# Kernel tuning notes

Measured on AMD Instinct MI355X. Metric: run time of the kernel, lower is better.

The kernel has to match this reference:

```python
import jax, jax.numpy as jnp
import numpy as np

# dims
B, S, IN, H = 8, 2048, 512, 512
# biophysical constants (from module defaults / buffers)
DT = 0.1
TAU_M, TAU_ADAPT = 20.0, 100.0
V_REST, V_THRESH, V_RESET = -65.0, -50.0, -65.0
ADAPT_A, ADAPT_B = 0.5, 0.1
E_NA, E_K, E_L = 50.0, -77.0, -54.4
# HH gate initial values (IonicCurrents lazy init)
M0, H0, N0 = 0.05, 0.6, 0.32


def setup_inputs() -> dict:
    key = jax.random.key(0)
    k1, k2 = jax.random.split(key)
    x = jax.random.normal(k1, (B, S, IN), dtype=jnp.float32)
    W = jax.random.normal(k2, (H, IN), dtype=jnp.float32) * 0.01  # SynapticPlasticity.weights
    return {
        "x": x,
        "W": W,
        "g_Na": jnp.float32(120.0),
        "g_K": jnp.float32(36.0),
        "g_L": jnp.float32(0.3),
    }


def reference(x, W, g_Na, g_K, g_L):
    """BiologicalSNNLayer.forward, first call (all internal states at init).

    post_spikes = psp0 = 0 and traces start at 0, so the STDP dw is exactly 0
    on this call; psp = 0*decay + syn_input = syn_input.
    """
    dt = jnp.float32(DT)
    # SynapticPlasticity forward output: F.linear(x, W)
    syn = jnp.einsum("bsi,hi->bsh", x, W)  # [B,S,H]
    psp = syn
    V = psp
    # Hodgkin-Huxley gating: one Euler step from initial gate values
    am = 0.1 * (V + 40.0) / (1.0 - jnp.exp(-(V + 40.0) / 10.0))
    bm = 4.0 * jnp.exp(-(V + 65.0) / 18.0)
    ah = 0.07 * jnp.exp(-(V + 65.0) / 20.0)
    bh = 1.0 / (1.0 + jnp.exp(-(V + 35.0) / 10.0))
    an = 0.01 * (V + 55.0) / (1.0 - jnp.exp(-(V + 55.0) / 10.0))
    bn = 0.125 * jnp.exp(-(V + 65.0) / 80.0)
    m = M0 + dt * (am * (1.0 - M0) - bm * M0)
    h = H0 + dt * (ah * (1.0 - H0) - bh * H0)
    n = N0 + dt * (an * (1.0 - N0) - bn * N0)
    I_ion = (
        g_Na * m ** 3 * h * (V - E_NA)
        + g_K * n ** 4 * (V - E_K)
        + g_L * (V - E_L)
    )
    # Adaptive LIF (all hidden_size neurons share params -> vectorized over last dim)
    I_in = I_ion + psp
    # v0 = V_REST, w0 = 0 -> dv = I_in * dt/tau_m
    v_new = V_REST + I_in * (dt / TAU_M)
    spike = (v_new >= V_THRESH).astype(jnp.float32)
    w_new = (ADAPT_A * (v_new - V_REST) + ADAPT_B * spike) * (dt / TAU_ADAPT)
    v_rs = jnp.where(spike > 0.5, jnp.float32(V_RESET), v_new)
    return spike, v_rs, w_new
```

## Files before the change

### kernel.cpp

```cpp
#include <hip/hip_runtime.h>
#include <hip/hip_bf16.h>
#include <math.h>

typedef __bf16 bf16x8 __attribute__((ext_vector_type(8)));
typedef float  f32x4  __attribute__((ext_vector_type(4)));

#define M_DIM 16384
#define N_DIM 512
#define K_DIM 512
#define TBL_N 1024

#define X_ELEMS ((long)M_DIM * K_DIM)
#define W_ELEMS ((long)N_DIM * K_DIM)
#define WS_NEED ((X_ELEMS + W_ELEMS) * 2)

__global__ __launch_bounds__(256)
void convert_kernel(const float* __restrict__ x, const float* __restrict__ W,
                    __bf16* __restrict__ xb, __bf16* __restrict__ wb)
{
    const long XN8 = X_ELEMS / 8;
    const long T8  = XN8 + W_ELEMS / 8;
    for (long i = (long)blockIdx.x * 256 + threadIdx.x; i < T8;
         i += (long)gridDim.x * 256) {
        const float* src;
        __bf16* dst;
        if (i < XN8) { src = x + i * 8;          dst = xb + i * 8; }
        else         { src = W + (i - XN8) * 8;  dst = wb + (i - XN8) * 8; }
        float4 a = *(const float4*)src;
        float4 b = *(const float4*)(src + 4);
        bf16x8 r;
        r[0] = (__bf16)a.x; r[1] = (__bf16)a.y; r[2] = (__bf16)a.z; r[3] = (__bf16)a.w;
        r[4] = (__bf16)b.x; r[5] = (__bf16)b.y; r[6] = (__bf16)b.z; r[7] = (__bf16)b.w;
        *(bf16x8*)dst = r;
    }
}

__device__ inline void gl_lds16(const __bf16* g, __bf16* l) {
    __builtin_amdgcn_global_load_lds(
        (const __attribute__((address_space(1))) void*)g,
        (__attribute__((address_space(3))) void*)l, 16, 0, 0);
}

__global__ __launch_bounds__(256, 4)
void gemm_hh_kernel(const __bf16* __restrict__ xb, const __bf16* __restrict__ wb,
                    const float* __restrict__ gNa_p, const float* __restrict__ gK_p,
                    const float* __restrict__ gL_p, float* __restrict__ out)
{
    __shared__ __bf16 sW[64 * 64];
    __shared__ __bf16 sX[128 * 64];
    __shared__ float  tbl[TBL_N + 1];

    const int tid = threadIdx.x;

    const int id   = blockIdx.x;
    const int xcd  = id & 7;
    const int slot = id >> 3;
    const int bm   = xcd * 16 + (slot >> 3);
    const int bn   = slot & 7;

    const int wv   = tid >> 6;
    const int ln   = tid & 63;
    const int lr   = ln & 15;
    const int quad = ln >> 4;

    const int rw  = ln >> 3;
    const int ch  = ln & 7;
    const int chx = (ch ^ rw) * 8;
    const __bf16* wSrc = wb + ((long)bn * 64 + 16 * wv + rw) * K_DIM + chx;
    const __bf16* xSrc = xb + ((long)bm * 128 + 32 * wv + rw) * K_DIM + chx;

    #pragma unroll
    for (int j = 0; j < 2; ++j)
        gl_lds16(wSrc + (long)(8 * j) * K_DIM, sW + (16 * wv + 8 * j) * 64);
    #pragma unroll
    for (int j = 0; j < 4; ++j)
        gl_lds16(xSrc + (long)(8 * j) * K_DIM, sX + (32 * wv + 8 * j) * 64);

    {
        const float gNa = *gNa_p, gK = *gK_p, gL = *gL_p;
        for (int i = tid; i <= TBL_N; i += 256) {
            const float V = -4.0f + (8.0f / TBL_N) * i;
            const float am = 0.1f * (V + 40.0f) / (1.0f - expf(-(V + 40.0f) * 0.1f));
            const float bm_ = 4.0f * expf(-(V + 65.0f) * (1.0f / 18.0f));
            const float ah = 0.07f * expf(-(V + 65.0f) * 0.05f);
            const float bh = 1.0f / (1.0f + expf(-(V + 35.0f) * 0.1f));
            const float an = 0.01f * (V + 55.0f) / (1.0f - expf(-(V + 55.0f) * 0.1f));
            const float bn_ = 0.125f * expf(-(V + 65.0f) * 0.0125f);
            const float m = 0.05f + 0.1f * (am * 0.95f - bm_ * 0.05f);
            const float h = 0.60f + 0.1f * (ah * 0.40f - bh * 0.60f);
            const float n = 0.32f + 0.1f * (an * 0.68f - bn_ * 0.32f);
            tbl[i] = gNa * m * m * m * h * (V - 50.0f)
                   + gK * (n * n) * (n * n) * (V + 77.0f)
                   + gL * (V + 54.4f) + V;
        }
    }
    __syncthreads();

    f32x4 acc[4][2] = {};

    for (int t = 0; t < 8; ++t) {
        #pragma unroll
        for (int kk = 0; kk < 2; ++kk) {
            const int cidx = quad + 4 * kk;
            const int sl   = (cidx ^ (lr & 7)) * 8;
            bf16x8 aw[4], bx[2];
            #pragma unroll
            for (int f = 0; f < 4; ++f)
                aw[f] = *(const bf16x8*)(sW + (f * 16 + lr) * 64 + sl);
            #pragma unroll
            for (int g = 0; g < 2; ++g)
                bx[g] = *(const bf16x8*)(sX + (32 * wv + g * 16 + lr) * 64 + sl);
            #pragma unroll
            for (int f = 0; f < 4; ++f)
                #pragma unroll
                for (int g = 0; g < 2; ++g)
                    acc[f][g] = __builtin_amdgcn_mfma_f32_16x16x32_bf16(
                        aw[f], bx[g], acc[f][g], 0, 0, 0);
        }
        if (t < 7) {
            __syncthreads();
            const int kt = (t + 1) * 64;
            #pragma unroll
            for (int j = 0; j < 2; ++j)
                gl_lds16(wSrc + (long)(8 * j) * K_DIM + kt, sW + (16 * wv + 8 * j) * 64);
            #pragma unroll
            for (int j = 0; j < 4; ++j)
                gl_lds16(xSrc + (long)(8 * j) * K_DIM + kt, sX + (32 * wv + 8 * j) * 64);
            __syncthreads();
        }
    }

    float* outS = out;
    float* outV = out + (long)M_DIM * N_DIM;
    float* outW = out + 2L * M_DIM * N_DIM;

    #pragma unroll
    for (int f = 0; f < 4; ++f) {
        const int gn4 = bn * 64 + f * 16 + quad * 4;
        #pragma unroll
        for (int g = 0; g < 2; ++g) {
            const long gm  = (long)bm * 128 + 32 * wv + g * 16 + lr;
            const long idx = gm * N_DIM + gn4;
            f32x4 vS, vV, vW;
            #pragma unroll
            for (int i = 0; i < 4; ++i) {
                const float V = acc[f][g][i];
                float u = (V + 4.0f) * (TBL_N / 8.0f);
                u = fminf(fmaxf(u, 0.0f), (float)TBL_N - 0.001f);
                const int   iu = (int)u;
                const float fr = u - (float)iu;
                const float I_in = tbl[iu] + fr * (tbl[iu + 1] - tbl[iu]);
                const float v_new = -65.0f + I_in * 0.005f;
                const float spike = (v_new >= -50.0f) ? 1.0f : 0.0f;
                vS[i] = spike;
                vW[i] = (0.5f * (v_new + 65.0f) + 0.1f * spike) * 0.001f;
                vV[i] = (spike > 0.5f) ? -65.0f : v_new;
            }
            *(f32x4*)(outS + idx) = vS;
            *(f32x4*)(outV + idx) = vV;
            *(f32x4*)(outW + idx) = vW;
        }
    }
}

#define BMf 64
#define BNf 128
#define LDSTf 72
typedef __bf16 bf16x4 __attribute__((ext_vector_type(4)));
__global__ __launch_bounds__(256, 4)
void snn_fallback_kernel(const float* __restrict__ x, const float* __restrict__ W,
                         const float* __restrict__ gNa_p, const float* __restrict__ gK_p,
                         const float* __restrict__ gL_p, float* __restrict__ out)
{
    __shared__ __bf16 sA[BMf * LDSTf];
    __shared__ __bf16 sB[BNf * LDSTf];
    __shared__ float  tbl[TBL_N + 1];

    const int tid = threadIdx.x;
    const int id   = blockIdx.x;
    const int xcd  = id & 7;
    const int slot = id >> 3;
    const int bm   = xcd * 32 + (slot >> 2);
    const int bn   = slot & 3;

    const int c4 = (tid & 15) * 4;
    const int r0 = tid >> 4;
    const float* xBase = x + (long)(bm * BMf + r0) * K_DIM + c4;
    const float* wBase = W + (long)(bn * BNf + r0) * K_DIM + c4;

    const int wave = tid >> 6;
    const int lane = tid & 63;
    const int wM   = (wave & 1) * 32;
    const int wN   = (wave >> 1) * 64;
    const int lr   = lane & 15;
    const int quad = lane >> 4;

    f32x4 acc[2][4] = {};
    float4 pa[4], pb[8];
    #pragma unroll
    for (int rr = 0; rr < 4; ++rr) pa[rr] = *(const float4*)(xBase + (long)rr * 16 * K_DIM);
    #pragma unroll
    for (int rr = 0; rr < 8; ++rr) pb[rr] = *(const float4*)(wBase + (long)rr * 16 * K_DIM);

    {
        const float gNa = *gNa_p, gK = *gK_p, gL = *gL_p;
        for (int i = tid; i <= TBL_N; i += 256) {
            const float V = -4.0f + (8.0f / TBL_N) * i;
            const float am = 0.1f * (V + 40.0f) / (1.0f - expf(-(V + 40.0f) * 0.1f));
            const float bm_ = 4.0f * expf(-(V + 65.0f) * (1.0f / 18.0f));
            const float ah = 0.07f * expf(-(V + 65.0f) * 0.05f);
            const float bh = 1.0f / (1.0f + expf(-(V + 35.0f) * 0.1f));
            const float an = 0.01f * (V + 55.0f) / (1.0f - expf(-(V + 55.0f) * 0.1f));
            const float bn_ = 0.125f * expf(-(V + 65.0f) * 0.0125f);
            const float m = 0.05f + 0.1f * (am * 0.95f - bm_ * 0.05f);
            const float h = 0.60f + 0.1f * (ah * 0.40f - bh * 0.60f);
            const float n = 0.32f + 0.1f * (an * 0.68f - bn_ * 0.32f);
            tbl[i] = gNa * m * m * m * h * (V - 50.0f)
                   + gK * (n * n) * (n * n) * (V + 77.0f)
                   + gL * (V + 54.4f) + V;
        }
    }

    for (int kt = 0; kt < K_DIM; kt += 64) {
        const int ktn = (kt + 64 < K_DIM) ? kt + 64 : kt;
        const float* xp = xBase + ktn;
        const float* wp = wBase + ktn;
        #pragma unroll
        for (int rr = 0; rr < 4; ++rr) {
            float4 v = pa[rr];
            pa[rr] = *(const float4*)(xp + (long)rr * 16 * K_DIM);
            bf16x4 b = { (__bf16)v.x, (__bf16)v.y, (__bf16)v.z, (__bf16)v.w };
            *(bf16x4*)(&sA[(r0 + rr * 16) * LDSTf + c4]) = b;
        }
        #pragma unroll
        for (int rr = 0; rr < 8; ++rr) {
            float4 v = pb[rr];
            pb[rr] = *(const float4*)(wp + (long)rr * 16 * K_DIM);
            bf16x4 b = { (__bf16)v.x, (__bf16)v.y, (__bf16)v.z, (__bf16)v.w };
            *(bf16x4*)(&sB[(r0 + rr * 16) * LDSTf + c4]) = b;
        }
        __syncthreads();
        #pragma unroll
        for (int ks = 0; ks < 64; ks += 32) {
            bf16x8 af[2], bfr[4];
            #pragma unroll
            for (int t = 0; t < 2; ++t)
                af[t]  = *(const bf16x8*)(&sA[(wM + t * 16 + lr) * LDSTf + ks + quad * 8]);
            #pragma unroll
            for (int t = 0; t < 4; ++t)
                bfr[t] = *(const bf16x8*)(&sB[(wN + t * 16 + lr) * LDSTf + ks + quad * 8]);
            #pragma unroll
            for (int mt = 0; mt < 2; ++mt)
                #pragma unroll
                for (int nt = 0; nt < 4; ++nt)
                    acc[mt][nt] = __builtin_amdgcn_mfma_f32_16x16x32_bf16(
                        af[mt], bfr[nt], acc[mt][nt], 0, 0, 0);
        }
        __syncthreads();
    }

    float* outS = out;
    float* outV = out + (long)M_DIM * N_DIM;
    float* outW = out + 2L * M_DIM * N_DIM;
    #pragma unroll
    for (int mt = 0; mt < 2; ++mt) {
        #pragma unroll
        for (int i = 0; i < 4; ++i) {
            const long gm = (long)bm * BMf + wM + mt * 16 + quad * 4 + i;
            #pragma unroll
            for (int nt = 0; nt < 4; ++nt) {
                const int gn = bn * BNf + wN + nt * 16 + lr;
                const float V = acc[mt][nt][i];
                float u = (V + 4.0f) * (TBL_N / 8.0f);
                u = fminf(fmaxf(u, 0.0f), (float)TBL_N - 0.001f);
                const int   iu = (int)u;
                const float f  = u - (float)iu;
                const float I_in = tbl[iu] + f * (tbl[iu + 1] - tbl[iu]);
                const float v_new = -65.0f + I_in * 0.005f;
                const float spike = (v_new >= -50.0f) ? 1.0f : 0.0f;
                const float w_new = (0.5f * (v_new + 65.0f) + 0.1f * spike) * 0.001f;
                const float v_rs  = (spike > 0.5f) ? -65.0f : v_new;
                const long idx = gm * N_DIM + gn;
                outS[idx] = spike; outV[idx] = v_rs; outW[idx] = w_new;
            }
        }
    }
}

extern "C" void kernel_launch(void* const* d_in, const int* in_sizes, int n_in,
                              void* d_out, int out_size, void* d_ws, size_t ws_size,
                              hipStream_t stream) {
    const float* x   = (const float*)d_in[0];
    const float* W   = (const float*)d_in[1];
    const float* gNa = (const float*)d_in[2];
    const float* gK  = (const float*)d_in[3];
    const float* gL  = (const float*)d_in[4];
    float* out = (float*)d_out;

    if (ws_size >= (size_t)WS_NEED) {
        __bf16* xb = (__bf16*)d_ws;
        __bf16* wb = xb + X_ELEMS;
        hipLaunchKernelGGL(convert_kernel, dim3(1024), dim3(256), 0, stream, x, W, xb, wb);
        hipLaunchKernelGGL(gemm_hh_kernel, dim3(1024), dim3(256), 0, stream,
                           xb, wb, gNa, gK, gL, out);
    } else {
        hipLaunchKernelGGL(snn_fallback_kernel, dim3(1024), dim3(256), 0, stream,
                           x, W, gNa, gK, gL, out);
    }
}
```

Measured before the change: 149.0 us.

## Fuse fp32-to-bf16 conversion into GEMM with register-prefetched loads

Drops the separate conversion kernel that wrote bf16 copies of x and W to the workspace. The GEMM now reads fp32 directly, keeps the next k-tile in registers while the current one is computed, and converts to bf16 on the way into LDS. This removes a full extra read and write pass over x and a second launch. In exchange each block reads twice as many bytes per tile, uses more registers for the prefetch buffers, and gives up the direct global-to-LDS load path.

Measured after the change: 178.8 us. 1.2x slower.

```diff
diff --git a/kernel.cpp b/kernel.cpp
--- a/kernel.cpp
+++ b/kernel.cpp
@@ -10,41 +10,17 @@
 #define K_DIM 512
 #define TBL_N 1024
 
-#define X_ELEMS ((long)M_DIM * K_DIM)
-#define W_ELEMS ((long)N_DIM * K_DIM)
-#define WS_NEED ((X_ELEMS + W_ELEMS) * 2)
-
-__global__ __launch_bounds__(256)
-void convert_kernel(const float* __restrict__ x, const float* __restrict__ W,
-                    __bf16* __restrict__ xb, __bf16* __restrict__ wb)
-{
-    const long XN8 = X_ELEMS / 8;
-    const long T8  = XN8 + W_ELEMS / 8;
-    for (long i = (long)blockIdx.x * 256 + threadIdx.x; i < T8;
-         i += (long)gridDim.x * 256) {
-        const float* src;
-        __bf16* dst;
-        if (i < XN8) { src = x + i * 8;          dst = xb + i * 8; }
-        else         { src = W + (i - XN8) * 8;  dst = wb + (i - XN8) * 8; }
-        float4 a = *(const float4*)src;
-        float4 b = *(const float4*)(src + 4);
-        bf16x8 r;
-        r[0] = (__bf16)a.x; r[1] = (__bf16)a.y; r[2] = (__bf16)a.z; r[3] = (__bf16)a.w;
-        r[4] = (__bf16)b.x; r[5] = (__bf16)b.y; r[6] = (__bf16)b.z; r[7] = (__bf16)b.w;
-        *(bf16x8*)dst = r;
-    }
-}
-
-__device__ inline void gl_lds16(const __bf16* g, __bf16* l) {
-    __builtin_amdgcn_global_load_lds(
-        (const __attribute__((address_space(1))) void*)g,
-        (__attribute__((address_space(3))) void*)l, 16, 0, 0);
+__device__ inline bf16x8 cvt8(float4 a, float4 b) {
+    bf16x8 r;
+    r[0] = (__bf16)a.x; r[1] = (__bf16)a.y; r[2] = (__bf16)a.z; r[3] = (__bf16)a.w;
+    r[4] = (__bf16)b.x; r[5] = (__bf16)b.y; r[6] = (__bf16)b.z; r[7] = (__bf16)b.w;
+    return r;
 }
 
 __global__ __launch_bounds__(256, 4)
-void gemm_hh_kernel(const __bf16* __restrict__ xb, const __bf16* __restrict__ wb,
-                    const float* __restrict__ gNa_p, const float* __restrict__ gK_p,
-                    const float* __restrict__ gL_p, float* __restrict__ out)
+void snn_fused_kernel(const float* __restrict__ x, const float* __restrict__ W,
+                      const float* __restrict__ gNa_p, const float* __restrict__ gK_p,
+                      const float* __restrict__ gL_p, float* __restrict__ out)
 {
     __shared__ __bf16 sW[64 * 64];
     __shared__ __bf16 sX[128 * 64];
@@ -66,15 +42,23 @@
     const int rw  = ln >> 3;
     const int ch  = ln & 7;
     const int chx = (ch ^ rw) * 8;
-    const __bf16* wSrc = wb + ((long)bn * 64 + 16 * wv + rw) * K_DIM + chx;
-    const __bf16* xSrc = xb + ((long)bm * 128 + 32 * wv + rw) * K_DIM + chx;
 
+    const float* wSrc = W + ((long)bn * 64 + 16 * wv + rw) * K_DIM + chx;
+    const float* xSrc = x + ((long)bm * 128 + 32 * wv + rw) * K_DIM + chx;
+    __bf16* wDst = sW + (16 * wv + rw) * 64 + ch * 8;
+    __bf16* xDst = sX + (32 * wv + rw) * 64 + ch * 8;
+
+    float4 pw[2][2], px[4][2];
     #pragma unroll
-    for (int j = 0; j < 2; ++j)
-        gl_lds16(wSrc + (long)(8 * j) * K_DIM, sW + (16 * wv + 8 * j) * 64);
+    for (int j = 0; j < 2; ++j) {
+        pw[j][0] = *(const float4*)(wSrc + (long)(8 * j) * K_DIM);
+        pw[j][1] = *(const float4*)(wSrc + (long)(8 * j) * K_DIM + 4);
+    }
     #pragma unroll
-    for (int j = 0; j < 4; ++j)
-        gl_lds16(xSrc + (long)(8 * j) * K_DIM, sX + (32 * wv + 8 * j) * 64);
+    for (int j = 0; j < 4; ++j) {
+        px[j][0] = *(const float4*)(xSrc + (long)(8 * j) * K_DIM);
+        px[j][1] = *(const float4*)(xSrc + (long)(8 * j) * K_DIM + 4);
+    }
 
     {
         const float gNa = *gNa_p, gK = *gK_p, gL = *gL_p;
@@ -94,11 +78,30 @@
                    + gL * (V + 54.4f) + V;
         }
     }
-    __syncthreads();
 
     f32x4 acc[4][2] = {};
 
     for (int t = 0; t < 8; ++t) {
+        const int nk = (t + 1) * 64;
+        #pragma unroll
+        for (int j = 0; j < 2; ++j) {
+            float4 a = pw[j][0], b = pw[j][1];
+            if (t < 7) {
+                pw[j][0] = *(const float4*)(wSrc + (long)(8 * j) * K_DIM + nk);
+                pw[j][1] = *(const float4*)(wSrc + (long)(8 * j) * K_DIM + nk + 4);
+            }
+            *(bf16x8*)(wDst + 8 * j * 64) = cvt8(a, b);
+        }
+        #pragma unroll
+        for (int j = 0; j < 4; ++j) {
+            float4 a = px[j][0], b = px[j][1];
+            if (t < 7) {
+                px[j][0] = *(const float4*)(xSrc + (long)(8 * j) * K_DIM + nk);
+                px[j][1] = *(const float4*)(xSrc + (long)(8 * j) * K_DIM + nk + 4);
+            }
+            *(bf16x8*)(xDst + 8 * j * 64) = cvt8(a, b);
+        }
+        __syncthreads();
         #pragma unroll
         for (int kk = 0; kk < 2; ++kk) {
             const int cidx = quad + 4 * kk;
@@ -117,17 +120,7 @@
                     acc[f][g] = __builtin_amdgcn_mfma_f32_16x16x32_bf16(
                         aw[f], bx[g], acc[f][g], 0, 0, 0);
         }
-        if (t < 7) {
-            __syncthreads();
-            const int kt = (t + 1) * 64;
-            #pragma unroll
-            for (int j = 0; j < 2; ++j)
-                gl_lds16(wSrc + (long)(8 * j) * K_DIM + kt, sW + (16 * wv + 8 * j) * 64);
-            #pragma unroll
-            for (int j = 0; j < 4; ++j)
-                gl_lds16(xSrc + (long)(8 * j) * K_DIM + kt, sX + (32 * wv + 8 * j) * 64);
-            __syncthreads();
-        }
+        __syncthreads();
     }
 
     float* outS = out;
@@ -163,130 +156,6 @@
     }
 }
 
-#define BMf 64
-#define BNf 128
-#define LDSTf 72
-typedef __bf16 bf16x4 __attribute__((ext_vector_type(4)));
-__global__ __launch_bounds__(256, 4)
-void snn_fallback_kernel(const float* __restrict__ x, const float* __restrict__ W,
-                         const float* __restrict__ gNa_p, const float* __restrict__ gK_p,
-                         const float* __restrict__ gL_p, float* __restrict__ out)
-{
-    __shared__ __bf16 sA[BMf * LDSTf];
-    __shared__ __bf16 sB[BNf * LDSTf];
-    __shared__ float  tbl[TBL_N + 1];
-
-    const int tid = threadIdx.x;
-    const int id   = blockIdx.x;
-    const int xcd  = id & 7;
-    const int slot = id >> 3;
-    const int bm   = xcd * 32 + (slot >> 2);
-    const int bn   = slot & 3;
-
-    const int c4 = (tid & 15) * 4;
-    const int r0 = tid >> 4;
-    const float* xBase = x + (long)(bm * BMf + r0) * K_DIM + c4;
-    const float* wBase = W + (long)(bn * BNf + r0) * K_DIM + c4;
-
-    const int wave = tid >> 6;
-    const int lane = tid & 63;
-    const int wM   = (wave & 1) * 32;
-    const int wN   = (wave >> 1) * 64;
-    const int lr   = lane & 15;
-    const int quad = lane >> 4;
-
-    f32x4 acc[2][4] = {};
-    float4 pa[4], pb[8];
-    #pragma unroll
-    for (int rr = 0; rr < 4; ++rr) pa[rr] = *(const float4*)(xBase + (long)rr * 16 * K_DIM);
-    #pragma unroll
-    for (int rr = 0; rr < 8; ++rr) pb[rr] = *(const float4*)(wBase + (long)rr * 16 * K_DIM);
-
-    {
-        const float gNa = *gNa_p, gK = *gK_p, gL = *gL_p;
-        for (int i = tid; i <= TBL_N; i += 256) {
-            const float V = -4.0f + (8.0f / TBL_N) * i;
-            const float am = 0.1f * (V + 40.0f) / (1.0f - expf(-(V + 40.0f) * 0.1f));
-            const float bm_ = 4.0f * expf(-(V + 65.0f) * (1.0f / 18.0f));
-            const float ah = 0.07f * expf(-(V + 65.0f) * 0.05f);
-            const float bh = 1.0f / (1.0f + expf(-(V + 35.0f) * 0.1f));
-            const float an = 0.01f * (V + 55.0f) / (1.0f - expf(-(V + 55.0f) * 0.1f));
-            const float bn_ = 0.125f * expf(-(V + 65.0f) * 0.0125f);
-            const float m = 0.05f + 0.1f * (am * 0.95f - bm_ * 0.05f);
-            const float h = 0.60f + 0.1f * (ah * 0.40f - bh * 0.60f);
-            const float n = 0.32f + 0.1f * (an * 0.68f - bn_ * 0.32f);
-            tbl[i] = gNa * m * m * m * h * (V - 50.0f)
-                   + gK * (n * n) * (n * n) * (V + 77.0f)
-                   + gL * (V + 54.4f) + V;
-        }
-    }
-
-    for (int kt = 0; kt < K_DIM; kt += 64) {
-        const int ktn = (kt + 64 < K_DIM) ? kt + 64 : kt;
-        const float* xp = xBase + ktn;
-        const float* wp = wBase + ktn;
-        #pragma unroll
-        for (int rr = 0; rr < 4; ++rr) {
-            float4 v = pa[rr];
-            pa[rr] = *(const float4*)(xp + (long)rr * 16 * K_DIM);
-            bf16x4 b = { (__bf16)v.x, (__bf16)v.y, (__bf16)v.z, (__bf16)v.w };
-            *(bf16x4*)(&sA[(r0 + rr * 16) * LDSTf + c4]) = b;
-        }
-        #pragma unroll
-        for (int rr = 0; rr < 8; ++rr) {
-            float4 v = pb[rr];
-            pb[rr] = *(const float4*)(wp + (long)rr * 16 * K_DIM);
-            bf16x4 b = { (__bf16)v.x, (__bf16)v.y, (__bf16)v.z, (__bf16)v.w };
-            *(bf16x4*)(&sB[(r0 + rr * 16) * LDSTf + c4]) = b;
-        }
-        __syncthreads();
-        #pragma unroll
-        for (int ks = 0; ks < 64; ks += 32) {
-            bf16x8 af[2], bfr[4];
-            #pragma unroll
-            for (int t = 0; t < 2; ++t)
-                af[t]  = *(const bf16x8*)(&sA[(wM + t * 16 + lr) * LDSTf + ks + quad * 8]);
-            #pragma unroll
-            for (int t = 0; t < 4; ++t)
-                bfr[t] = *(const bf16x8*)(&sB[(wN + t * 16 + lr) * LDSTf + ks + quad * 8]);
-            #pragma unroll
-            for (int mt = 0; mt < 2; ++mt)
-                #pragma unroll
-                for (int nt = 0; nt < 4; ++nt)
-                    acc[mt][nt] = __builtin_amdgcn_mfma_f32_16x16x32_bf16(
-                        af[mt], bfr[nt], acc[mt][nt], 0, 0, 0);
-        }
-        __syncthreads();
-    }
-
-    float* outS = out;
-    float* outV = out + (long)M_DIM * N_DIM;
-    float* outW = out + 2L * M_DIM * N_DIM;
-    #pragma unroll
-    for (int mt = 0; mt < 2; ++mt) {
-        #pragma unroll
-        for (int i = 0; i < 4; ++i) {
-            const long gm = (long)bm * BMf + wM + mt * 16 + quad * 4 + i;
-            #pragma unroll
-            for (int nt = 0; nt < 4; ++nt) {
-                const int gn = bn * BNf + wN + nt * 16 + lr;
-                const float V = acc[mt][nt][i];
-                float u = (V + 4.0f) * (TBL_N / 8.0f);
-                u = fminf(fmaxf(u, 0.0f), (float)TBL_N - 0.001f);
-                const int   iu = (int)u;
-                const float f  = u - (float)iu;
-                const float I_in = tbl[iu] + f * (tbl[iu + 1] - tbl[iu]);
-                const float v_new = -65.0f + I_in * 0.005f;
-                const float spike = (v_new >= -50.0f) ? 1.0f : 0.0f;
-                const float w_new = (0.5f * (v_new + 65.0f) + 0.1f * spike) * 0.001f;
-                const float v_rs  = (spike > 0.5f) ? -65.0f : v_new;
-                const long idx = gm * N_DIM + gn;
-                outS[idx] = spike; outV[idx] = v_rs; outW[idx] = w_new;
-            }
-        }
-    }
-}
-
 extern "C" void kernel_launch(void* const* d_in, const int* in_sizes, int n_in,
                               void* d_out, int out_size, void* d_ws, size_t ws_size,
                               hipStream_t stream) {
@@ -296,15 +165,8 @@
     const float* gK  = (const float*)d_in[3];
     const float* gL  = (const float*)d_in[4];
     float* out = (float*)d_out;
+    (void)d_ws; (void)ws_size;
 
-    if (ws_size >= (size_t)WS_NEED) {
-        __bf16* xb = (__bf16*)d_ws;
-        __bf16* wb = xb + X_ELEMS;
-        hipLaunchKernelGGL(convert_kernel, dim3(1024), dim3(256), 0, stream, x, W, xb, wb);
-        hipLaunchKernelGGL(gemm_hh_kernel, dim3(1024), dim3(256), 0, stream,
-                           xb, wb, gNa, gK, gL, out);
-    } else {
-        hipLaunchKernelGGL(snn_fallback_kernel, dim3(1024), dim3(256), 0, stream,
-                           x, W, gNa, gK, gL, out);
-    }
+    hipLaunchKernelGGL(snn_fused_kernel, dim3(1024), dim3(256), 0, stream,
+                       x, W, gNa, gK, gL, out);
 }
```
